# Optimization experiments

Hardware: AMD Instinct MI355X
Metric: run time of the kernel (lower is better)

The kernel has to match this reference:

```python
import jax, jax.numpy as jnp
import numpy as np

B, N, IN_DIM, OUT_DIM, H = 8, 1024, 256, 256, 8
D = OUT_DIM // H  # support_dim = 32


def setup_inputs() -> dict:
    key = jax.random.key(0)
    k_a, k_x, k_w, k_f1, k_f2 = jax.random.split(key, 5)
    A = (jax.random.uniform(k_a, (B, N, N)) < 0.05).astype(jnp.float32)
    eye = jnp.eye(N, dtype=jnp.float32)
    A = jnp.maximum(A, eye[None, :, :])
    X = jax.random.normal(k_x, (B, N, IN_DIM), dtype=jnp.float32)
    std_w = 1.0 / np.sqrt(OUT_DIM)
    std_f = 1.0 / np.sqrt(D)
    weight = jax.random.uniform(k_w, (IN_DIM, OUT_DIM), minval=-std_w, maxval=std_w)
    fc1 = jax.random.uniform(k_f1, (H, D), minval=-std_f, maxval=std_f)
    fc2 = jax.random.uniform(k_f2, (H, D), minval=-std_f, maxval=std_f)
    return {"A": A, "X": X, "weight": weight, "fc1": fc1, "fc2": fc2}


def reference(A, X, weight, fc1, fc2):
    # inputs: [B, N, H, D]
    inputs = jnp.einsum('bni,io->bno', X, weight).reshape(B, N, H, D)
    # additive attention scores (rank-1 broadcast)
    self_s = jnp.einsum('bnhd,hd->bhn', inputs, fc1)   # [B,H,N] (query/self term)
    neigh_s = jnp.einsum('bnhd,hd->bhn', inputs, fc2)  # [B,H,N] (key/neighbor term)
    scores = jax.nn.leaky_relu(self_s[:, :, :, None] + neigh_s[:, :, None, :])  # [B,H,N,N]
    mask = (-1e9 * (1.0 - A))[:, None, :, :]  # [B,1,N,N]
    alphas = jax.nn.softmax(scores + mask, axis=-1)  # [B,H,N,N]
    out = jnp.einsum('bhnm,bmhd->bnhd', alphas, inputs).reshape(B, N, OUT_DIM)
    return jax.nn.relu(out)
```

## Files before the change

### kernel.cpp

```cpp
#include <hip/hip_runtime.h>

typedef unsigned short u16;
typedef __attribute__((ext_vector_type(8))) short short8;
typedef __attribute__((ext_vector_type(4))) float floatx4;

#define NB 8
#define NN 1024
#define KDIM 256
#define ODIM 256
#define NH 8
#define LDA 264
#define ECAP 256
#define ESTR 260

__device__ __forceinline__ u16 bf_rne(float x) {
    union { float f; unsigned u; } c{x};
    unsigned r = c.u + 0x7fff + ((c.u >> 16) & 1);
    return (u16)(r >> 16);
}
__device__ __forceinline__ float bf_f(u16 b) {
    union { unsigned u; float f; } c{(unsigned)b << 16};
    return c.f;
}
#define SPLIT1(val, A_, B_) { u16 hh_ = bf_rne(val); u16 ll_ = bf_rne((val) - bf_f(hh_)); A_ = hh_; B_ = ll_; }

__global__ __launch_bounds__(256) void wprep(const float* __restrict__ W,
                                             u16* __restrict__ WhiT,
                                             u16* __restrict__ WloT) {
    __shared__ float tile[64][65];
    int bt = blockIdx.x;
    int kt = bt >> 2, ot = bt & 3;
    int tid = threadIdx.x;
    int r = tid >> 6, c = tid & 63;
#pragma unroll
    for (int rr = r; rr < 64; rr += 4)
        tile[rr][c] = W[(kt * 64 + rr) * ODIM + ot * 64 + c];
    __syncthreads();
#pragma unroll
    for (int oo = r; oo < 64; oo += 4) {
        float w = tile[c][oo];
        u16 h, l;
        SPLIT1(w, h, l)
        WhiT[(ot * 64 + oo) * KDIM + kt * 64 + c] = h;
        WloT[(ot * 64 + oo) * KDIM + kt * 64 + c] = l;
    }
}

__global__ __launch_bounds__(256) void gemm_scores(
        const float* __restrict__ X, const u16* __restrict__ WhiT,
        const u16* __restrict__ WloT, const float* __restrict__ fc1,
        const float* __restrict__ fc2, u16* __restrict__ inp,
        float* __restrict__ self_s, float* __restrict__ neigh_s) {
    __shared__ u16 ah_lds[16 * LDA];
    __shared__ u16 al_lds[16 * LDA];

    int tid = threadIdx.x;
    int w = tid >> 6, lane = tid & 63;
    int m = lane & 15, q = lane >> 4;
    int row0 = blockIdx.x * 16;

    const float4* Xr = (const float4*)(X + (size_t)row0 * KDIM);
#pragma unroll
    for (int p = 0; p < 4; ++p) {
        int f = p * 256 + tid;
        int r = f >> 6, c4 = (f & 63) * 4;
        float4 v = Xr[f];
        ushort4 hi, lo;
        SPLIT1(v.x, hi.x, lo.x)
        SPLIT1(v.y, hi.y, lo.y)
        SPLIT1(v.z, hi.z, lo.z)
        SPLIT1(v.w, hi.w, lo.w)
        *(ushort4*)&ah_lds[r * LDA + c4] = hi;
        *(ushort4*)&al_lds[r * LDA + c4] = lo;
    }
    __syncthreads();

    floatx4 acc[4] = {{0,0,0,0},{0,0,0,0},{0,0,0,0},{0,0,0,0}};
#pragma unroll
    for (int k0 = 0; k0 < KDIM; k0 += 32) {
        short8 Ah = *(const short8*)&ah_lds[m * LDA + k0 + q * 8];
        short8 Al = *(const short8*)&al_lds[m * LDA + k0 + q * 8];
#pragma unroll
        for (int t = 0; t < 4; ++t) {
            int o = w * 64 + t * 16 + m;
            short8 Bh = *(const short8*)(WhiT + (size_t)o * KDIM + k0 + q * 8);
            short8 Bl = *(const short8*)(WloT + (size_t)o * KDIM + k0 + q * 8);
            acc[t] = __builtin_amdgcn_mfma_f32_16x16x32_bf16(Ah, Bh, acc[t], 0, 0, 0);
            acc[t] = __builtin_amdgcn_mfma_f32_16x16x32_bf16(Ah, Bl, acc[t], 0, 0, 0);
            acc[t] = __builtin_amdgcn_mfma_f32_16x16x32_bf16(Al, Bh, acc[t], 0, 0, 0);
        }
    }

#pragma unroll
    for (int t = 0; t < 4; ++t) {
        int col = w * 64 + t * 16 + m;
#pragma unroll
        for (int r = 0; r < 4; ++r)
            inp[(size_t)(row0 + q * 4 + r) * ODIM + col] = bf_rne(acc[t][r]);
    }

    float f1[4], f2[4];
#pragma unroll
    for (int t = 0; t < 4; ++t) {
        int col = w * 64 + t * 16 + m;
        f1[t] = fc1[col];
        f2[t] = fc2[col];
    }
#pragma unroll
    for (int r = 0; r < 4; ++r) {
        float a0 = acc[0][r] * f1[0] + acc[1][r] * f1[1];
        float b0 = acc[0][r] * f2[0] + acc[1][r] * f2[1];
        float a1 = acc[2][r] * f1[2] + acc[3][r] * f1[3];
        float b1 = acc[2][r] * f2[2] + acc[3][r] * f2[3];
#pragma unroll
        for (int ofs = 8; ofs >= 1; ofs >>= 1) {
            a0 += __shfl_xor(a0, ofs);
            b0 += __shfl_xor(b0, ofs);
            a1 += __shfl_xor(a1, ofs);
            b1 += __shfl_xor(b1, ofs);
        }
        if (m == 0) {
            int n = row0 + q * 4 + r;
            int b = n >> 10, nn = n & 1023;
            self_s [((size_t)(b * NH + 2 * w) << 10) + nn] = a0;
            neigh_s[((size_t)(b * NH + 2 * w) << 10) + nn] = b0;
            self_s [((size_t)(b * NH + 2 * w + 1) << 10) + nn] = a1;
            neigh_s[((size_t)(b * NH + 2 * w + 1) << 10) + nn] = b1;
        }
    }
}

__global__ __launch_bounds__(256) void gat_agg(
        const float* __restrict__ A, const u16* __restrict__ inp,
        const float* __restrict__ self_s, const float* __restrict__ neigh_s,
        float* __restrict__ out) {
    __shared__ u16 lst[NN];
    __shared__ float esc[NH][ESTR];
    __shared__ float red[4][256];
    __shared__ float hinv[NH];
    __shared__ int cnt;

    int bx = blockIdx.x;
    int b = bx & 7;
    int n = bx >> 3;
    int bn = (b << 10) | n;
    int tid = threadIdx.x;

    if (tid == 0) cnt = 0;
    __syncthreads();
    {
        float4 a4 = ((const float4*)(A + (size_t)bn * NN))[tid];
        int base = tid * 4;
        if (a4.x != 0.f) lst[atomicAdd(&cnt, 1)] = (u16)base;
        if (a4.y != 0.f) lst[atomicAdd(&cnt, 1)] = (u16)(base + 1);
        if (a4.z != 0.f) lst[atomicAdd(&cnt, 1)] = (u16)(base + 2);
        if (a4.w != 0.f) lst[atomicAdd(&cnt, 1)] = (u16)(base + 3);
    }
    __syncthreads();
    int nnz = cnt;
    if (nnz > ECAP) nnz = ECAP;

    int h = tid >> 5, j = tid & 31;
    const float* nsh = neigh_s + ((size_t)(b * NH + h) << 10);
    float selfv = self_s[((size_t)(b * NH + h) << 10) + n];
    float lsum = 0.f;
    for (int i = j; i < nnz; i += 32) {
        float s = selfv + nsh[lst[i]];
        s = s > 0.f ? s : 0.01f * s;
        float e = __expf(s);
        esc[h][i] = e;
        lsum += e;
    }
#pragma unroll
    for (int ofs = 16; ofs >= 1; ofs >>= 1)
        lsum += __shfl_xor(lsum, ofs);
    if (j == 0) hinv[h] = 1.f / lsum;
    __syncthreads();

    int wv = tid >> 6, lane = tid & 63;
    int hh = lane >> 3;
    const ushort4* ib = (const ushort4*)(inp + (((size_t)b) << 10) * ODIM) + lane;
    floatx4 acc = {0.f, 0.f, 0.f, 0.f};
#pragma unroll 4
    for (int i = wv; i < nnz; i += 4) {
        float e = esc[hh][i];
        ushort4 v = ib[(size_t)lst[i] * 64];
        acc[0] = fmaf(e, bf_f(v.x), acc[0]);
        acc[1] = fmaf(e, bf_f(v.y), acc[1]);
        acc[2] = fmaf(e, bf_f(v.z), acc[2]);
        acc[3] = fmaf(e, bf_f(v.w), acc[3]);
    }
    *(floatx4*)&red[wv][lane * 4] = acc;
    __syncthreads();

    float r0 = red[0][tid] + red[1][tid] + red[2][tid] + red[3][tid];
    r0 *= hinv[tid >> 5];
    out[(size_t)bn * ODIM + tid] = r0 > 0.f ? r0 : 0.f;
}

extern "C" void kernel_launch(void* const* d_in, const int* in_sizes, int n_in,
                              void* d_out, int out_size, void* d_ws, size_t ws_size,
                              hipStream_t stream) {
    const float* A   = (const float*)d_in[0];
    const float* X   = (const float*)d_in[1];
    const float* W   = (const float*)d_in[2];
    const float* fc1 = (const float*)d_in[3];
    const float* fc2 = (const float*)d_in[4];
    float* out = (float*)d_out;

    char* ws = (char*)d_ws;
    const size_t MB = 1024u * 1024u;
    u16*   inp     = (u16*)ws;
    u16*   WhiT    = (u16*)(ws + 4 * MB);
    u16*   WloT    = (u16*)(ws + 4 * MB + 128 * 1024);
    float* self_s  = (float*)(ws + 4 * MB + 256 * 1024);
    float* neigh_s = (float*)(ws + 4 * MB + 512 * 1024);

    wprep<<<16, 256, 0, stream>>>(W, WhiT, WloT);
    gemm_scores<<<NB * NN / 16, 256, 0, stream>>>(
        X, WhiT, WloT, fc1, fc2, inp, self_s, neigh_s);
    gat_agg<<<NB * NN, 256, 0, stream>>>(A, inp, self_s, neigh_s, out);
}
```

Measured before the change: 126.8 us.

## Retile score GEMM to 32-row tiles split over two column halves

The projection GEMM now gives each block 32 rows of X and one 128-column half of the output, so each wave computes a 2x2 grid of 16x16 tiles. Every loaded B fragment of the split-bf16 weights is reused across two row tiles, which halves global weight loads per MFMA. Each wave now owns exactly one head, which simplifies the score reduction. The cost is that X is loaded and split to hi/lo bf16 twice, once per column-half block, and LDS per block doubles.

After: 123.8 us. 2.4% less time.

```diff
diff --git a/kernel.cpp b/kernel.cpp
--- a/kernel.cpp
+++ b/kernel.cpp
@@ -9,6 +9,7 @@
 #define KDIM 256
 #define ODIM 256
 #define NH 8
+#define BR 32
 #define LDA 264
 #define ECAP 256
 #define ESTR 260
@@ -51,17 +52,19 @@
         const u16* __restrict__ WloT, const float* __restrict__ fc1,
         const float* __restrict__ fc2, u16* __restrict__ inp,
         float* __restrict__ self_s, float* __restrict__ neigh_s) {
-    __shared__ u16 ah_lds[16 * LDA];
-    __shared__ u16 al_lds[16 * LDA];
+    __shared__ u16 ah_lds[BR * LDA];
+    __shared__ u16 al_lds[BR * LDA];
 
     int tid = threadIdx.x;
     int w = tid >> 6, lane = tid & 63;
     int m = lane & 15, q = lane >> 4;
-    int row0 = blockIdx.x * 16;
+    int bid = blockIdx.x;
+    int row0 = (bid >> 1) * BR;
+    int cbase = (bid & 1) * 128;
 
     const float4* Xr = (const float4*)(X + (size_t)row0 * KDIM);
 #pragma unroll
-    for (int p = 0; p < 4; ++p) {
+    for (int p = 0; p < 8; ++p) {
         int f = p * 256 + tid;
         int r = f >> 6, c4 = (f & 63) * 4;
         float4 v = Xr[f];
@@ -75,59 +78,64 @@
     }
     __syncthreads();
 
-    floatx4 acc[4] = {{0,0,0,0},{0,0,0,0},{0,0,0,0},{0,0,0,0}};
+    floatx4 acc[2][2] = {{{0,0,0,0},{0,0,0,0}},{{0,0,0,0},{0,0,0,0}}};
 #pragma unroll
     for (int k0 = 0; k0 < KDIM; k0 += 32) {
-        short8 Ah = *(const short8*)&ah_lds[m * LDA + k0 + q * 8];
-        short8 Al = *(const short8*)&al_lds[m * LDA + k0 + q * 8];
-#pragma unroll
-        for (int t = 0; t < 4; ++t) {
-            int o = w * 64 + t * 16 + m;
+        short8 Ah0 = *(const short8*)&ah_lds[m * LDA + k0 + q * 8];
+        short8 Al0 = *(const short8*)&al_lds[m * LDA + k0 + q * 8];
+        short8 Ah1 = *(const short8*)&ah_lds[(16 + m) * LDA + k0 + q * 8];
+        short8 Al1 = *(const short8*)&al_lds[(16 + m) * LDA + k0 + q * 8];
+#pragma unroll
+        for (int t = 0; t < 2; ++t) {
+            int o = cbase + w * 32 + t * 16 + m;
             short8 Bh = *(const short8*)(WhiT + (size_t)o * KDIM + k0 + q * 8);
             short8 Bl = *(const short8*)(WloT + (size_t)o * KDIM + k0 + q * 8);
-            acc[t] = __builtin_amdgcn_mfma_f32_16x16x32_bf16(Ah, Bh, acc[t], 0, 0, 0);
-            acc[t] = __builtin_amdgcn_mfma_f32_16x16x32_bf16(Ah, Bl, acc[t], 0, 0, 0);
-            acc[t] = __builtin_amdgcn_mfma_f32_16x16x32_bf16(Al, Bh, acc[t], 0, 0, 0);
+            acc[0][t] = __builtin_amdgcn_mfma_f32_16x16x32_bf16(Ah0, Bh, acc[0][t], 0, 0, 0);
+            acc[0][t] = __builtin_amdgcn_mfma_f32_16x16x32_bf16(Ah0, Bl, acc[0][t], 0, 0, 0);
+            acc[0][t] = __builtin_amdgcn_mfma_f32_16x16x32_bf16(Al0, Bh, acc[0][t], 0, 0, 0);
+            acc[1][t] = __builtin_amdgcn_mfma_f32_16x16x32_bf16(Ah1, Bh, acc[1][t], 0, 0, 0);
+            acc[1][t] = __builtin_amdgcn_mfma_f32_16x16x32_bf16(Ah1, Bl, acc[1][t], 0, 0, 0);
+            acc[1][t] = __builtin_amdgcn_mfma_f32_16x16x32_bf16(Al1, Bh, acc[1][t], 0, 0, 0);
         }
     }
 
 #pragma unroll
-    for (int t = 0; t < 4; ++t) {
-        int col = w * 64 + t * 16 + m;
-#pragma unroll
-        for (int r = 0; r < 4; ++r)
-            inp[(size_t)(row0 + q * 4 + r) * ODIM + col] = bf_rne(acc[t][r]);
-    }
-
-    float f1[4], f2[4];
-#pragma unroll
-    for (int t = 0; t < 4; ++t) {
-        int col = w * 64 + t * 16 + m;
-        f1[t] = fc1[col];
-        f2[t] = fc2[col];
-    }
-#pragma unroll
-    for (int r = 0; r < 4; ++r) {
-        float a0 = acc[0][r] * f1[0] + acc[1][r] * f1[1];
-        float b0 = acc[0][r] * f2[0] + acc[1][r] * f2[1];
-        float a1 = acc[2][r] * f1[2] + acc[3][r] * f1[3];
-        float b1 = acc[2][r] * f2[2] + acc[3][r] * f2[3];
-#pragma unroll
-        for (int ofs = 8; ofs >= 1; ofs >>= 1) {
-            a0 += __shfl_xor(a0, ofs);
-            b0 += __shfl_xor(b0, ofs);
-            a1 += __shfl_xor(a1, ofs);
-            b1 += __shfl_xor(b1, ofs);
+    for (int rt = 0; rt < 2; ++rt)
+#pragma unroll
+        for (int t = 0; t < 2; ++t) {
+            int col = cbase + w * 32 + t * 16 + m;
+#pragma unroll
+            for (int r = 0; r < 4; ++r)
+                inp[(size_t)(row0 + rt * 16 + q * 4 + r) * ODIM + col] =
+                    bf_rne(acc[rt][t][r]);
         }
-        if (m == 0) {
-            int n = row0 + q * 4 + r;
-            int b = n >> 10, nn = n & 1023;
-            self_s [((size_t)(b * NH + 2 * w) << 10) + nn] = a0;
-            neigh_s[((size_t)(b * NH + 2 * w) << 10) + nn] = b0;
-            self_s [((size_t)(b * NH + 2 * w + 1) << 10) + nn] = a1;
-            neigh_s[((size_t)(b * NH + 2 * w + 1) << 10) + nn] = b1;
+
+    int hd = (bid & 1) * 4 + w;
+    float f1[2], f2[2];
+#pragma unroll
+    for (int t = 0; t < 2; ++t) {
+        int cl = hd * 32 + t * 16 + m;
+        f1[t] = fc1[cl];
+        f2[t] = fc2[cl];
+    }
+#pragma unroll
+    for (int rt = 0; rt < 2; ++rt)
+#pragma unroll
+        for (int r = 0; r < 4; ++r) {
+            float a = acc[rt][0][r] * f1[0] + acc[rt][1][r] * f1[1];
+            float bb = acc[rt][0][r] * f2[0] + acc[rt][1][r] * f2[1];
+#pragma unroll
+            for (int ofs = 8; ofs >= 1; ofs >>= 1) {
+                a += __shfl_xor(a, ofs);
+                bb += __shfl_xor(bb, ofs);
+            }
+            if (m == 0) {
+                int n = row0 + rt * 16 + q * 4 + r;
+                int b = n >> 10, nn = n & 1023;
+                self_s [((size_t)(b * NH + hd) << 10) + nn] = a;
+                neigh_s[((size_t)(b * NH + hd) << 10) + nn] = bb;
+            }
         }
-    }
 }
 
 __global__ __launch_bounds__(256) void gat_agg(
@@ -217,7 +225,7 @@
     float* neigh_s = (float*)(ws + 4 * MB + 512 * 1024);
 
     wprep<<<16, 256, 0, stream>>>(W, WhiT, WloT);
-    gemm_scores<<<NB * NN / 16, 256, 0, stream>>>(
+    gemm_scores<<<(NB * NN / BR) * 2, 256, 0, stream>>>(
         X, WhiT, WloT, fc1, fc2, inp, self_s, neigh_s);
     gat_agg<<<NB * NN, 256, 0, stream>>>(A, inp, self_s, neigh_s, out);
 }
```
